# Kernel optimization log

Measured on AMD Instinct MI355X. Metric: run time of the kernel, lower is better.

Reference implementation:

```python
import jax, jax.numpy as jnp
import numpy as np

H, ND, RD, VD = 16, 128, 64, 128  # heads, nope/rope/v head dims
EPS = 1e-6


def rmsnorm(x, g):
    return x * jax.lax.rsqrt(jnp.mean(x * x, axis=-1, keepdims=True) + EPS) * g


def apply_rope(x, cos, sin):
    # x: [B,T,h,D]; cos/sin: [1,T,1,D/2]; interleaved pair rotation
    x1, x2 = x[..., 0::2], x[..., 1::2]
    o1 = x1 * cos - x2 * sin
    o2 = x1 * sin + x2 * cos
    return jnp.stack([o1, o2], axis=-1).reshape(x.shape)


def setup_inputs() -> dict:
    key = jax.random.key(0)
    ks = jax.random.split(key, 10)
    B, T, D = 2, 2048, 2048
    QR, KVR = 1536, 512
    s = 0.02
    return {
        "x": jax.random.normal(ks[0], (B, T, D), jnp.float32),
        "w_cq": jax.random.normal(ks[1], (D, QR), jnp.float32) * s,
        "g_q": jnp.ones((QR,), jnp.float32),
        "w_ckv": jax.random.normal(ks[2], (D, KVR), jnp.float32) * s,
        "g_kv": jnp.ones((KVR,), jnp.float32),
        "w_dq_nope": jax.random.normal(ks[3], (QR, H * ND), jnp.float32) * s,
        "w_dq_rope": jax.random.normal(ks[4], (QR, H * RD), jnp.float32) * s,
        "w_dk_nope": jax.random.normal(ks[5], (KVR, H * ND), jnp.float32) * s,
        "w_dv": jax.random.normal(ks[6], (KVR, H * VD), jnp.float32) * s,
        "w_k_rope": jax.random.normal(ks[7], (D, RD), jnp.float32) * s,
        "w_out": jax.random.normal(ks[8], (H * VD, D), jnp.float32) * s,
    }


def reference(x, w_cq, g_q, w_ckv, g_kv, w_dq_nope, w_dq_rope,
              w_dk_nope, w_dv, w_k_rope, w_out):
    B, T, D = x.shape
    # low-rank latents + RMSNorm
    q_lat = rmsnorm(x @ w_cq, g_q)          # [B,T,QR]
    kv_lat = rmsnorm(x @ w_ckv, g_kv)        # [B,T,KVR]
    q_nope = (q_lat @ w_dq_nope).reshape(B, T, H, ND)
    q_rope = (q_lat @ w_dq_rope).reshape(B, T, H, RD)
    k_nope = (kv_lat @ w_dk_nope).reshape(B, T, H, ND)
    v = (kv_lat @ w_dv).reshape(B, T, H, VD)
    k_rope = (x @ w_k_rope).reshape(B, T, 1, RD)  # shared across heads
    # RoPE (start_pos = 0, no past_kv)
    pos = jnp.arange(T, dtype=jnp.float32)
    inv_freq = 1.0 / (10000.0 ** (jnp.arange(0, RD, 2, dtype=jnp.float32) / RD))
    ang = pos[:, None] * inv_freq[None, :]               # [T, RD/2]
    cos = jnp.cos(ang)[None, :, None, :]
    sin = jnp.sin(ang)[None, :, None, :]
    q_rope = apply_rope(q_rope, cos, sin)
    k_rope = apply_rope(k_rope, cos, sin)
    k_rope = jnp.broadcast_to(k_rope, (B, T, H, RD))
    q = jnp.concatenate([q_nope, q_rope], axis=-1).transpose(0, 2, 1, 3)  # [B,H,T,ND+RD]
    k = jnp.concatenate([k_nope, k_rope], axis=-1).transpose(0, 2, 1, 3)
    v_t = v.transpose(0, 2, 1, 3)                                        # [B,H,T,VD]
    # causal SDPA, scale = 1/sqrt(head_dim)
    scale = 1.0 / jnp.sqrt(jnp.asarray(ND + RD, jnp.float32))
    scores = jnp.einsum('bhqd,bhkd->bhqk', q, k) * scale
    causal = jnp.tril(jnp.ones((T, T), dtype=bool))
    scores = jnp.where(causal[None, None], scores, -jnp.inf)
    attn = jax.nn.softmax(scores, axis=-1)
    out = jnp.einsum('bhqk,bhkd->bhqd', attn, v_t)
    out = out.transpose(0, 2, 1, 3).reshape(B, T, H * VD) @ w_out        # [B,T,D]
    return out, k, v_t
```

## Files before the change

### kernel.cpp

```cpp
#include <hip/hip_runtime.h>
#include <cstdint>
#include <cstddef>

typedef _Float16 HT;
typedef _Float16 h8 __attribute__((ext_vector_type(8)));
typedef _Float16 h4 __attribute__((ext_vector_type(4)));
typedef float f32x4 __attribute__((ext_vector_type(4)));

constexpr int Tn  = 2048;
constexpr int Dm  = 2048;
constexpr int Hh  = 16;
constexpr int RDc = 64;
constexpr int QRc = 1536;
constexpr int KVRc= 512;
constexpr int BT  = 4096;

#define VWAIT(N) asm volatile("s_waitcnt vmcnt(" #N ")" ::: "memory")
#define SBAR()   __builtin_amdgcn_s_barrier()

__device__ __forceinline__ f32x4 mfma16(h8 a, h8 b, f32x4 c) {
    return __builtin_amdgcn_mfma_f32_16x16x32_f16(a, b, c, 0, 0, 0);
}
__device__ __forceinline__ void gload_lds16(const void* g, void* l) {
    __builtin_amdgcn_global_load_lds(
        (const __attribute__((address_space(1))) unsigned int*)g,
        (__attribute__((address_space(3))) unsigned int*)l, 16, 0, 0);
}

__global__ __launch_bounds__(256)
void cstab_kernel(float2* __restrict__ cs)
{
    const int idx = blockIdx.x * 256 + threadIdx.x;
    const int t = idx >> 5, i = idx & 31;
    const float ang = (float)t * exp2f(-(float)i * (13.287712379549449f / 32.f));
    cs[idx] = make_float2(cosf(ang), sinf(ang));
}

struct WT8 {
    const float* s[8];
    HT* d[8];
    int K[8], N[8], start[8];
};

__global__ __launch_bounds__(256)
void wtrans8_kernel(WT8 p)
{
    __shared__ float Ts[64][65];
    int seg = 0;
    #pragma unroll
    for (int i = 1; i < 8; i++) if ((int)blockIdx.x >= p.start[i]) seg = i;
    const float* src = p.s[seg];
    HT* dst = p.d[seg];
    const int K = p.K[seg], N = p.N[seg];
    const int bx = blockIdx.x - p.start[seg];
    const int nx = N >> 6;
    const int n0 = (bx % nx) * 64, k0 = (bx / nx) * 64;
    const int tid = threadIdx.x;
    {
        const int r = tid >> 2, c0 = (tid & 3) * 16;
        const float* s = src + (size_t)(k0 + r) * N + n0 + c0;
        #pragma unroll
        for (int j = 0; j < 4; j++)
            *reinterpret_cast<f32x4*>(&Ts[r][c0 + j * 4]) = *reinterpret_cast<const f32x4*>(s + j * 4);
    }
    __syncthreads();
    {
        const int c = tid >> 2, kq = (tid & 3) * 16;
        h8 o0, o1;
        #pragma unroll
        for (int j = 0; j < 8; j++) { o0[j] = (HT)Ts[kq + j][c]; o1[j] = (HT)Ts[kq + 8 + j][c]; }
        HT* d = dst + (size_t)(n0 + c) * K + k0 + kq;
        *reinterpret_cast<h8*>(d)     = o0;
        *reinterpret_cast<h8*>(d + 8) = o1;
    }
}

__global__ __launch_bounds__(256)
void convx_kernel(const float* __restrict__ x, HT* __restrict__ x16)
{
    const size_t i = ((size_t)blockIdx.x * 256 + threadIdx.x) * 8;
    f32x4 a = *reinterpret_cast<const f32x4*>(x + i);
    f32x4 b = *reinterpret_cast<const f32x4*>(x + i + 4);
    h8 v;
    #pragma unroll
    for (int j = 0; j < 4; j++) { v[j] = (HT)a[j]; v[4 + j] = (HT)b[j]; }
    *reinterpret_cast<h8*>(x16 + i) = v;
}

template<int EPI>
__global__ __launch_bounds__(256)
void gemm16d(const HT* __restrict__ A, const HT* __restrict__ Bt, const int K,
             HT* __restrict__ o1, HT* __restrict__ o2, HT* __restrict__ o3,
             float* __restrict__ f1, float* __restrict__ f2,
             const float2* __restrict__ cstab)
{
    __shared__ HT As[2][4096];
    __shared__ HT Bs[2][4096];

    const int tid  = threadIdx.x;
    const int lane = tid & 63;
    const int l15  = lane & 15, l4 = lane >> 4;
    const int w    = tid >> 6;
    const int wr   = w >> 1, wc = w & 1;
    const int m0   = blockIdx.y * 128;
    const int n0   = blockIdx.x * 128;

    f32x4 acc[4][4] = {};
    const int nk = K >> 5;

    const int schunk = ((lane & 3) ^ ((lane >> 2) & 3) ^ ((lane >> 4) & 3)) * 8;

#define GSTAGE(as_, bs_, kt_) do {                                             \
    _Pragma("unroll")                                                          \
    for (int i_ = 0; i_ < 2; i_++) {                                           \
        const int row_ = (w * 2 + i_) * 16 + (lane >> 2);                      \
        gload_lds16(A  + (size_t)(m0 + row_) * K + (kt_) + schunk,             \
                    (as_) + (w * 2 + i_) * 512);                               \
        gload_lds16(Bt + (size_t)(n0 + row_) * K + (kt_) + schunk,             \
                    (bs_) + (w * 2 + i_) * 512);                               \
    } } while (0)

    GSTAGE(As[0], Bs[0], 0);

    const int sl = (l4 ^ (l15 & 3) ^ ((l15 >> 2) & 3)) * 8;

    for (int kt = 0; kt < nk; kt++) {
        HT* as = As[kt & 1];
        HT* bs = Bs[kt & 1];
        if (kt + 1 < nk) {
            GSTAGE(As[(kt + 1) & 1], Bs[(kt + 1) & 1], (kt + 1) * 32);
            VWAIT(4);
        } else {
            VWAIT(0);
        }
        SBAR();

        h8 af[4], bf[4];
        #pragma unroll
        for (int f = 0; f < 4; f++)
            af[f] = *reinterpret_cast<const h8*>(&as[(wr * 64 + f * 16 + l15) * 32 + sl]);
        #pragma unroll
        for (int g = 0; g < 4; g++)
            bf[g] = *reinterpret_cast<const h8*>(&bs[(wc * 64 + g * 16 + l15) * 32 + sl]);
        #pragma unroll
        for (int f = 0; f < 4; f++)
            #pragma unroll
            for (int g = 0; g < 4; g++)
                acc[f][g] = mfma16(af[f], bf[g], acc[f][g]);
        SBAR();
    }
#undef GSTAGE

    #pragma unroll
    for (int f = 0; f < 4; f++) {
        #pragma unroll
        for (int g = 0; g < 4; g++) {
            const int row = m0 + wr * 64 + f * 16 + l4 * 4;
            const int col = n0 + wc * 64 + g * 16 + l15;
            if constexpr (EPI == 3) {
                #pragma unroll
                for (int r = 0; r < 4; r++)
                    f1[(size_t)(row + r) * 2048 + col] = acc[f][g][r];
            } else if constexpr (EPI == 0) {
                if (col < 1536) {
                    #pragma unroll
                    for (int r = 0; r < 4; r++)
                        o1[(size_t)(row + r) * 1536 + col] = (HT)acc[f][g][r];
                } else if (col < 2048) {
                    #pragma unroll
                    for (int r = 0; r < 4; r++)
                        o2[(size_t)(row + r) * 512 + (col - 1536)] = (HT)acc[f][g][r];
                } else if (col < 2112) {
                    const int cc = col - 2048;
                    const int i = cc >> 1;
                    const bool odd = cc & 1;
                    #pragma unroll
                    for (int r = 0; r < 4; r++) {
                        const int t = (row + r) & (Tn - 1);
                        const float2 cs = cstab[t * 32 + i];
                        const float v = acc[f][g][r];
                        const float p = __shfl_xor(v, 1);
                        const float ov = odd ? p * cs.y + v * cs.x : v * cs.x - p * cs.y;
                        o3[(size_t)(row + r) * 64 + cc] = (HT)ov;
                    }
                }
            } else if constexpr (EPI == 1) {
                if (col < 2048) {
                    #pragma unroll
                    for (int r = 0; r < 4; r++)
                        o1[(size_t)(row + r) * 2048 + col] = (HT)acc[f][g][r];
                } else {
                    const int cc = col - 2048;
                    const int i = (cc & 63) >> 1;
                    const bool odd = cc & 1;
                    #pragma unroll
                    for (int r = 0; r < 4; r++) {
                        const int t = (row + r) & (Tn - 1);
                        const float2 cs = cstab[t * 32 + i];
                        const float v = acc[f][g][r];
                        const float p = __shfl_xor(v, 1);
                        const float ov = odd ? p * cs.y + v * cs.x : v * cs.x - p * cs.y;
                        o2[(size_t)(row + r) * 1024 + cc] = (HT)ov;
                    }
                }
            } else {
                if (col < 2048) {
                    const int h = col >> 7, d = col & 127;
                    #pragma unroll
                    for (int r = 0; r < 4; r++) {
                        const int rw = row + r;
                        const int b = rw >> 11, t = rw & (Tn - 1);
                        o1[(size_t)rw * 2048 + col] = (HT)acc[f][g][r];
                        f1[((size_t)(b * Hh + h) * Tn + t) * 192 + d] = acc[f][g][r];
                    }
                } else {
                    const int c2 = col - 2048;
                    const int h = c2 >> 7, d = c2 & 127;
                    const int b = row >> 11, t0 = row & (Tn - 1);
                    h4 pk;
                    #pragma unroll
                    for (int r = 0; r < 4; r++) {
                        f2[((size_t)(b * Hh + h) * Tn + t0 + r) * 128 + d] = acc[f][g][r];
                        pk[r] = (HT)acc[f][g][r];
                    }
                    *reinterpret_cast<h4*>(&o3[((size_t)(b * Hh + h) * 128 + d) * Tn + t0]) = pk;
                }
            }
        }
    }
}

__global__ __launch_bounds__(256)
void kropebc_kernel(const HT* __restrict__ kr16, float* __restrict__ out_k)
{
    const int idx = blockIdx.x * 256 + threadIdx.x;
    const int j4 = (idx & 15) * 4;
    const int t  = (idx >> 4) & (Tn - 1);
    const int b  = idx >> 15;
    h4 v = *reinterpret_cast<const h4*>(&kr16[((size_t)(b * Tn + t)) * 64 + j4]);
    f32x4 f;
    #pragma unroll
    for (int r = 0; r < 4; r++) f[r] = (float)v[r];
    #pragma unroll
    for (int h = 0; h < Hh; h++)
        *reinterpret_cast<f32x4*>(&out_k[((size_t)(b * Hh + h) * Tn + t) * 192 + 128 + j4]) = f;
}

__global__ __launch_bounds__(256)
void rmsnorm2_kernel(HT* __restrict__ Xa, const float* __restrict__ ga,
                     HT* __restrict__ Xb, const float* __restrict__ gb)
{
    const int which = blockIdx.y;
    HT* X = which ? Xb : Xa;
    const float* g = which ? gb : ga;
    const int N = which ? 512 : 1536;
    const int row = blockIdx.x;
    HT* x = X + (size_t)row * N;
    float ss = 0.f;
    for (int i = threadIdx.x * 8; i < N; i += 2048) {
        h8 v = *reinterpret_cast<const h8*>(&x[i]);
        #pragma unroll
        for (int j = 0; j < 8; j++) { float f = (float)v[j]; ss += f * f; }
    }
    #pragma unroll
    for (int sh = 32; sh >= 1; sh >>= 1) ss += __shfl_xor(ss, sh);
    __shared__ float red[4];
    if ((threadIdx.x & 63) == 0) red[threadIdx.x >> 6] = ss;
    __syncthreads();
    const float tot = red[0] + red[1] + red[2] + red[3];
    const float scale = rsqrtf(tot / (float)N + 1e-6f);
    for (int i = threadIdx.x * 8; i < N; i += 2048) {
        h8 v = *reinterpret_cast<const h8*>(&x[i]);
        f32x4 g0 = *reinterpret_cast<const f32x4*>(&g[i]);
        f32x4 g1 = *reinterpret_cast<const f32x4*>(&g[i + 4]);
        #pragma unroll
        for (int j = 0; j < 4; j++) { v[j]   = (HT)((float)v[j]   * scale * g0[j]);
                                      v[4+j] = (HT)((float)v[4+j] * scale * g1[j]); }
        *reinterpret_cast<h8*>(&x[i]) = v;
    }
}

__global__ __launch_bounds__(256, 2)
void attn10_kernel(const HT* __restrict__ qn, const HT* __restrict__ qr,
                   const HT* __restrict__ kn, const HT* __restrict__ kr16,
                   const HT* __restrict__ vt, HT* __restrict__ ao)
{
    __shared__ HT Ks_n[2][32 * 128];
    __shared__ HT Ks_r[2][32 * 64];
    __shared__ HT Vs[2][128 * 32];
    __shared__ HT Ps[4][32][40];

    const int tid  = threadIdx.x;
    const int lane = tid & 63;
    const int l15  = lane & 15, l4 = lane >> 4;
    const int w    = tid >> 6;

    const int bid = blockIdx.x;
    const int j   = bid >> 5;
    const int h   = bid & 15;
    const int b   = (bid >> 4) & 1;
    const int thi = 31 - j;

    const size_t bT = (size_t)b * Tn;
    const HT* vt_h = vt + ((size_t)(b * Hh + h) * 128) * Tn;

    const int qw0 = j   * 64 + w * 16;
    const int qw1 = thi * 64 + w * 16;

    h8 aq0[6], aq1[6];
    {
        const HT sc = (HT)(0.07216878364870323f * 1.4426950408889634f);
        const size_t rq0 = bT + qw0 + l15;
        const HT* pn = qn + rq0 * 2048 + h * 128 + l4 * 8;
        #pragma unroll
        for (int f = 0; f < 4; f++) aq0[f] = *reinterpret_cast<const h8*>(pn + f * 32) * sc;
        const HT* pr = qr + rq0 * 1024 + h * 64 + l4 * 8;
        aq0[4] = *reinterpret_cast<const h8*>(pr) * sc;
        aq0[5] = *reinterpret_cast<const h8*>(pr + 32) * sc;
        const size_t rq1 = bT + qw1 + l15;
        const HT* pn1 = qn + rq1 * 2048 + h * 128 + l4 * 8;
        #pragma unroll
        for (int f = 0; f < 4; f++) aq1[f] = *reinterpret_cast<const h8*>(pn1 + f * 32) * sc;
        const HT* pr1 = qr + rq1 * 1024 + h * 64 + l4 * 8;
        aq1[4] = *reinterpret_cast<const h8*>(pr1) * sc;
        aq1[5] = *reinterpret_cast<const h8*>(pr1 + 32) * sc;
    }

    f32x4 o0[8] = {}, o1[8] = {};
    float m0v[4] = {-1e30f, -1e30f, -1e30f, -1e30f};
    float m1v[4] = {-1e30f, -1e30f, -1e30f, -1e30f};
    float l0v[4] = {0.f, 0.f, 0.f, 0.f};
    float l1v[4] = {0.f, 0.f, 0.f, 0.f};

#define STAGE(sl_, kb_) do {                                                    \
    _Pragma("unroll")                                                           \
    for (int jj = 0; jj < 2; jj++) {                                            \
        const int cc = w * 2 + jj;                                              \
        const int r_ = cc * 4 + (lane >> 4);                                    \
        const int cl = (l15 & 8) | ((l15 & 7) ^ (r_ & 7));                      \
        gload_lds16(kn + (bT + (kb_) + r_) * 2048 + h * 128 + cl * 8,           \
                    &Ks_n[sl_][cc * 512]);                                      \
    }                                                                           \
    {                                                                           \
        const int r_ = w * 8 + (lane >> 3);                                     \
        const int cl = (lane & 7) ^ (r_ & 7);                                   \
        gload_lds16(kr16 + (bT + (kb_) + r_) * 64 + cl * 8,                     \
                    &Ks_r[sl_][w * 512]);                                       \
    }                                                                           \
    _Pragma("unroll")                                                           \
    for (int jj = 0; jj < 2; jj++) {                                            \
        const int cc = w * 2 + jj;                                              \
        const int d_ = cc * 16 + (lane >> 2);                                   \
        const int cl = (lane & 3) ^ (d_ & 3);                                   \
        gload_lds16(vt_h + (size_t)d_ * Tn + (kb_) + cl * 8,                    \
                    &Vs[sl_][cc * 512]);                                        \
    } } while (0)

#define SMX(sv, mv, lv, ov, qwx, prow)                                          \
{                                                                               \
    float a_[4][2]; float mxr_[4]; bool ok_ = true;                             \
    _Pragma("unroll")                                                           \
    for (int r = 0; r < 4; r++) {                                               \
        const int qrow = (qwx) + l4 * 4 + r;                                    \
        _Pragma("unroll")                                                       \
        for (int c = 0; c < 2; c++)                                             \
            a_[r][c] = (kb + c * 16 + l15 <= qrow) ? sv[c][r] : -1e30f;         \
        mxr_[r] = fmaxf(a_[r][0], a_[r][1]);                                    \
        ok_ = ok_ && (mxr_[r] <= mv[r] + 8.f);                                  \
    }                                                                           \
    if (__builtin_expect((bool)__all(ok_), 1)) {                                \
        _Pragma("unroll")                                                       \
        for (int r = 0; r < 4; r++) {                                           \
            float rs = 0.f;                                                     \
            _Pragma("unroll")                                                   \
            for (int c = 0; c < 2; c++) {                                       \
                const float e = __builtin_exp2f(a_[r][c] - mv[r]);              \
                rs += e;                                                        \
                Ps[w][(prow) + l4 * 4 + r][c * 16 + l15] = (HT)e;               \
            }                                                                   \
            lv[r] += rs;                                                        \
        }                                                                       \
    } else {                                                                    \
        float al_[4];                                                           \
        _Pragma("unroll")                                                       \
        for (int r = 0; r < 4; r++) {                                           \
            float mx = mxr_[r];                                                 \
            _Pragma("unroll")                                                   \
            for (int sh = 1; sh < 16; sh <<= 1) mx = fmaxf(mx, __shfl_xor(mx, sh)); \
            const float mn = fmaxf(mv[r], mx);                                  \
            al_[r] = __builtin_exp2f(mv[r] - mn);                               \
            mv[r] = mn;                                                         \
            float rs = 0.f;                                                     \
            _Pragma("unroll")                                                   \
            for (int c = 0; c < 2; c++) {                                       \
                const float e = __builtin_exp2f(a_[r][c] - mn);                 \
                rs += e;                                                        \
                Ps[w][(prow) + l4 * 4 + r][c * 16 + l15] = (HT)e;               \
            }                                                                   \
            lv[r] = lv[r] * al_[r] + rs;                                        \
        }                                                                       \
        _Pragma("unroll")                                                       \
        for (int g = 0; g < 8; g++)                                             \
            _Pragma("unroll")                                                   \
            for (int r = 0; r < 4; r++) ov[g][r] *= al_[r];                     \
    }                                                                           \
}

#define KBODY(ACT0)                                                             \
{                                                                               \
    f32x4 s0[2] = {}, s1[2] = {};                                               \
    __builtin_amdgcn_s_setprio(1);                                              \
    _Pragma("unroll")                                                           \
    for (int c = 0; c < 2; c++) {                                               \
        const int kr = c * 16 + l15;                                            \
        const int sw = (kr & 7) << 4;                                           \
        const char* kbase = (const char*)&Ks_n[sl][0] + kr * 256;               \
        const char* rbase = (const char*)&Ks_r[sl][0] + kr * 128;               \
        const h8 br0 = *(const h8*)(rbase + ((l4 * 16) ^ sw));                  \
        const h8 br1 = *(const h8*)(rbase + ((64 + l4 * 16) ^ sw));             \
        _Pragma("unroll")                                                       \
        for (int f = 0; f < 4; f++) {                                           \
            const h8 kf = *(const h8*)(kbase + ((f * 64 + l4 * 16) ^ sw));      \
            s1[c] = mfma16(aq1[f], kf, s1[c]);                                  \
            if (ACT0) s0[c] = mfma16(aq0[f], kf, s0[c]);                        \
        }                                                                       \
        s1[c] = mfma16(aq1[4], br0, s1[c]);                                     \
        s1[c] = mfma16(aq1[5], br1, s1[c]);                                     \
        if (ACT0) { s0[c] = mfma16(aq0[4], br0, s0[c]);                         \
                    s0[c] = mfma16(aq0[5], br1, s0[c]); }                       \
    }                                                                           \
    __builtin_amdgcn_s_setprio(0);                                              \
    SMX(s1, m1v, l1v, o1, qw1, 16);                                             \
    if (ACT0) SMX(s0, m0v, l0v, o0, qw0, 0);                                    \
    const h8 ap1 = *reinterpret_cast<const h8*>(&Ps[w][16 + l15][l4 * 8]);      \
    h8 ap0 = ap1;                                                               \
    if (ACT0) ap0 = *reinterpret_cast<const h8*>(&Ps[w][l15][l4 * 8]);          \
    __builtin_amdgcn_s_setprio(1);                                              \
    _Pragma("unroll")                                                           \
    for (int g = 0; g < 8; g++) {                                               \
        const int d = g * 16 + l15;                                             \
        const int swd = (d & 3) << 4;                                           \
        const char* vbase = (const char*)&Vs[sl][0] + d * 64;                   \
        const h8 v0 = *(const h8*)(vbase + ((l4 * 16) ^ swd));                  \
        o1[g] = mfma16(ap1, v0, o1[g]);                                         \
        if (ACT0) o0[g] = mfma16(ap0, v0, o0[g]);                               \
    }                                                                           \
    __builtin_amdgcn_s_setprio(0);                                              \
}

    const int nkb = (thi + 1) * 2;
    STAGE(0, 0);

    for (int t = 0; t < nkb; t++) {
        const int kb = t * 32;
        const int sl = t & 1;
        if (t + 1 < nkb) {
            STAGE(sl ^ 1, kb + 32);
            VWAIT(5);
        } else {
            VWAIT(0);
        }
        SBAR();
        if (kb <= qw0 + 15)      KBODY(1)
        else if (kb <= qw1 + 15) KBODY(0)
        SBAR();
    }
#undef KBODY
#undef SMX
#undef STAGE

    {
        const size_t orow = bT + qw1 + l4 * 4;
        #pragma unroll
        for (int r = 0; r < 4; r++) {
            float rsum = l1v[r];
            #pragma unroll
            for (int sh = 1; sh < 16; sh <<= 1) rsum += __shfl_xor(rsum, sh);
            const float inv = 1.0f / rsum;
            HT* dst = ao + (orow + r) * 2048 + h * 128 + l15;
            #pragma unroll
            for (int g = 0; g < 8; g++) dst[g * 16] = (HT)(o1[g][r] * inv);
        }
    }
    {
        const size_t orow = bT + qw0 + l4 * 4;
        #pragma unroll
        for (int r = 0; r < 4; r++) {
            float rsum = l0v[r];
            #pragma unroll
            for (int sh = 1; sh < 16; sh <<= 1) rsum += __shfl_xor(rsum, sh);
            const float inv = 1.0f / rsum;
            HT* dst = ao + (orow + r) * 2048 + h * 128 + l15;
            #pragma unroll
            for (int g = 0; g < 8; g++) dst[g * 16] = (HT)(o0[g][r] * inv);
        }
    }
}

extern "C" void kernel_launch(void* const* d_in, const int* in_sizes, int n_in,
                              void* d_out, int out_size, void* d_ws, size_t ws_size,
                              hipStream_t stream)
{
    const float* x     = (const float*)d_in[0];
    const float* w_cq  = (const float*)d_in[1];
    const float* g_q   = (const float*)d_in[2];
    const float* w_ckv = (const float*)d_in[3];
    const float* g_kv  = (const float*)d_in[4];
    const float* w_dqn = (const float*)d_in[5];
    const float* w_dqr = (const float*)d_in[6];
    const float* w_dkn = (const float*)d_in[7];
    const float* w_dv  = (const float*)d_in[8];
    const float* w_kr  = (const float*)d_in[9];
    const float* w_out = (const float*)d_in[10];

    char* ws = (char*)d_ws;
    HT* cqT   = (HT*)(ws + 0);
    HT* ckvT  = (HT*)(ws + 6291456);
    HT* krT   = (HT*)(ws + 8388608);
    HT* dqnT  = (HT*)(ws + 8912896);
    HT* dqrT  = (HT*)(ws + 15204352);
    HT* dknT  = (HT*)(ws + 18350080);
    HT* dvT   = (HT*)(ws + 20447232);
    HT* outT  = (HT*)(ws + 22544384);
    HT* cq    = (HT*)(ws + 30932992);
    HT* ckv   = (HT*)(ws + 43515904);
    HT* qn    = (HT*)(ws + 47710208);
    HT* qr    = (HT*)(ws + 64487424);
    HT* kn    = (HT*)(ws + 72876032);
    HT* kr16  = (HT*)(ws + 89653248);
    HT* vt    = (HT*)(ws + 0);
    HT* x16   = qn;
    HT* ao    = qn;

    float* out_o = (float*)d_out;
    float* out_k = out_o + (size_t)BT * Dm;
    float* out_v = out_k + (size_t)2 * Hh * Tn * 192;
    float2* cstab = (float2*)out_v;

    const dim3 blk(256);

    cstab_kernel<<<dim3(256), blk, 0, stream>>>(cstab);

    WT8 wt;
    wt.s[0]=w_cq;  wt.d[0]=cqT;  wt.K[0]=2048; wt.N[0]=1536;
    wt.s[1]=w_ckv; wt.d[1]=ckvT; wt.K[1]=2048; wt.N[1]=512;
    wt.s[2]=w_kr;  wt.d[2]=krT;  wt.K[2]=2048; wt.N[2]=64;
    wt.s[3]=w_dqn; wt.d[3]=dqnT; wt.K[3]=1536; wt.N[3]=2048;
    wt.s[4]=w_dqr; wt.d[4]=dqrT; wt.K[4]=1536; wt.N[4]=1024;
    wt.s[5]=w_dkn; wt.d[5]=dknT; wt.K[5]=512;  wt.N[5]=2048;
    wt.s[6]=w_dv;  wt.d[6]=dvT;  wt.K[6]=512;  wt.N[6]=2048;
    wt.s[7]=w_out; wt.d[7]=outT; wt.K[7]=2048; wt.N[7]=2048;
    {
        int acc = 0;
        for (int i = 0; i < 8; i++) {
            wt.start[i] = acc;
            acc += (wt.N[i] >> 6) * (wt.K[i] >> 6);
        }
        wtrans8_kernel<<<dim3(acc), blk, 0, stream>>>(wt);
    }

    convx_kernel<<<dim3(4096), blk, 0, stream>>>(x, x16);

    gemm16d<0><<<dim3(17, BT/128), blk, 0, stream>>>(x16, cqT, Dm,
        cq, ckv, kr16, nullptr, nullptr, cstab);
    kropebc_kernel<<<dim3(256), blk, 0, stream>>>(kr16, out_k);

    rmsnorm2_kernel<<<dim3(BT, 2), blk, 0, stream>>>(cq, g_q, ckv, g_kv);

    gemm16d<1><<<dim3(24, BT/128), blk, 0, stream>>>(cq, dqnT, QRc,
        qn, qr, nullptr, nullptr, nullptr, cstab);
    gemm16d<2><<<dim3(32, BT/128), blk, 0, stream>>>(ckv, dknT, KVRc,
        kn, nullptr, vt, out_k, out_v, nullptr);

    attn10_kernel<<<dim3(512), blk, 0, stream>>>(qn, qr, kn, kr16, vt, ao);

    gemm16d<3><<<dim3(16, BT/128), blk, 0, stream>>>(ao, outT, Dm,
        nullptr, nullptr, nullptr, out_o, nullptr, nullptr);
}
```

Before: 340.8 us.

## Merge prep kernels into one launch, fuse k_rope broadcast into GEMM, retune V swizzle

Folds the cos/sin table, weight transpose and x-to-fp16 conversion into a single prep kernel dispatched by block-index range, which removes two launches. It also writes the roped k_rope broadcast to all 16 heads of the fp32 output directly from the first GEMM epilogue, so the separate broadcast kernel goes away. The V tile LDS swizzle in attention now uses (d>>1)&3 instead of d&3 to change the bank-conflict pattern. The new epilogue stores are scalar and strided rather than vectorized, and they lengthen the first GEMM.

```diff
diff --git a/kernel.cpp b/kernel.cpp
--- a/kernel.cpp
+++ b/kernel.cpp
@@ -27,35 +27,49 @@
         (__attribute__((address_space(3))) unsigned int*)l, 16, 0, 0);
 }
 
-__global__ __launch_bounds__(256)
-void cstab_kernel(float2* __restrict__ cs)
-{
-    const int idx = blockIdx.x * 256 + threadIdx.x;
-    const int t = idx >> 5, i = idx & 31;
-    const float ang = (float)t * exp2f(-(float)i * (13.287712379549449f / 32.f));
-    cs[idx] = make_float2(cosf(ang), sinf(ang));
-}
-
-struct WT8 {
+struct PrepArgs {
     const float* s[8];
     HT* d[8];
     int K[8], N[8], start[8];
+    float2* cs;
+    const float* x;
+    HT* x16;
 };
 
 __global__ __launch_bounds__(256)
-void wtrans8_kernel(WT8 p)
+void prep_kernel(PrepArgs p)
 {
     __shared__ float Ts[64][65];
+    const int bid = blockIdx.x;
+    const int tid = threadIdx.x;
+
+    if (bid < 256) {
+        const int idx = bid * 256 + tid;
+        const int t = idx >> 5, i = idx & 31;
+        const float ang = (float)t * exp2f(-(float)i * (13.287712379549449f / 32.f));
+        p.cs[idx] = make_float2(cosf(ang), sinf(ang));
+        return;
+    }
+    if (bid >= 4000) {
+        const size_t i = ((size_t)(bid - 4000) * 256 + tid) * 8;
+        f32x4 a = *reinterpret_cast<const f32x4*>(p.x + i);
+        f32x4 b = *reinterpret_cast<const f32x4*>(p.x + i + 4);
+        h8 v;
+        #pragma unroll
+        for (int j = 0; j < 4; j++) { v[j] = (HT)a[j]; v[4 + j] = (HT)b[j]; }
+        *reinterpret_cast<h8*>(p.x16 + i) = v;
+        return;
+    }
+    const int bx0 = bid - 256;
     int seg = 0;
     #pragma unroll
-    for (int i = 1; i < 8; i++) if ((int)blockIdx.x >= p.start[i]) seg = i;
+    for (int i = 1; i < 8; i++) if (bx0 >= p.start[i]) seg = i;
     const float* src = p.s[seg];
     HT* dst = p.d[seg];
     const int K = p.K[seg], N = p.N[seg];
-    const int bx = blockIdx.x - p.start[seg];
+    const int bx = bx0 - p.start[seg];
     const int nx = N >> 6;
     const int n0 = (bx % nx) * 64, k0 = (bx / nx) * 64;
-    const int tid = threadIdx.x;
     {
         const int r = tid >> 2, c0 = (tid & 3) * 16;
         const float* s = src + (size_t)(k0 + r) * N + n0 + c0;
@@ -73,18 +87,6 @@
         *reinterpret_cast<h8*>(d)     = o0;
         *reinterpret_cast<h8*>(d + 8) = o1;
     }
-}
-
-__global__ __launch_bounds__(256)
-void convx_kernel(const float* __restrict__ x, HT* __restrict__ x16)
-{
-    const size_t i = ((size_t)blockIdx.x * 256 + threadIdx.x) * 8;
-    f32x4 a = *reinterpret_cast<const f32x4*>(x + i);
-    f32x4 b = *reinterpret_cast<const f32x4*>(x + i + 4);
-    h8 v;
-    #pragma unroll
-    for (int j = 0; j < 4; j++) { v[j] = (HT)a[j]; v[4 + j] = (HT)b[j]; }
-    *reinterpret_cast<h8*>(x16 + i) = v;
 }
 
 template<int EPI>
@@ -176,12 +178,17 @@
                     const bool odd = cc & 1;
                     #pragma unroll
                     for (int r = 0; r < 4; r++) {
-                        const int t = (row + r) & (Tn - 1);
+                        const int rw = row + r;
+                        const int t = rw & (Tn - 1);
+                        const int b = rw >> 11;
                         const float2 cs = cstab[t * 32 + i];
                         const float v = acc[f][g][r];
                         const float p = __shfl_xor(v, 1);
                         const float ov = odd ? p * cs.y + v * cs.x : v * cs.x - p * cs.y;
-                        o3[(size_t)(row + r) * 64 + cc] = (HT)ov;
+                        o3[(size_t)rw * 64 + cc] = (HT)ov;
+                        #pragma unroll
+                        for (int hh = 0; hh < Hh; hh++)
+                            f1[((size_t)(b * Hh + hh) * Tn + t) * 192 + 128 + cc] = ov;
                     }
                 }
             } else if constexpr (EPI == 1) {
@@ -228,22 +235,6 @@
             }
         }
     }
-}
-
-__global__ __launch_bounds__(256)
-void kropebc_kernel(const HT* __restrict__ kr16, float* __restrict__ out_k)
-{
-    const int idx = blockIdx.x * 256 + threadIdx.x;
-    const int j4 = (idx & 15) * 4;
-    const int t  = (idx >> 4) & (Tn - 1);
-    const int b  = idx >> 15;
-    h4 v = *reinterpret_cast<const h4*>(&kr16[((size_t)(b * Tn + t)) * 64 + j4]);
-    f32x4 f;
-    #pragma unroll
-    for (int r = 0; r < 4; r++) f[r] = (float)v[r];
-    #pragma unroll
-    for (int h = 0; h < Hh; h++)
-        *reinterpret_cast<f32x4*>(&out_k[((size_t)(b * Hh + h) * Tn + t) * 192 + 128 + j4]) = f;
 }
 
 __global__ __launch_bounds__(256)
@@ -351,7 +342,7 @@
     for (int jj = 0; jj < 2; jj++) {                                            \
         const int cc = w * 2 + jj;                                              \
         const int d_ = cc * 16 + (lane >> 2);                                   \
-        const int cl = (lane & 3) ^ (d_ & 3);                                   \
+        const int cl = (lane & 3) ^ ((d_ >> 1) & 3);                            \
         gload_lds16(vt_h + (size_t)d_ * Tn + (kb_) + cl * 8,                    \
                     &Vs[sl_][cc * 512]);                                        \
     } } while (0)
@@ -439,7 +430,7 @@
     _Pragma("unroll")                                                           \
     for (int g = 0; g < 8; g++) {                                               \
         const int d = g * 16 + l15;                                             \
-        const int swd = (d & 3) << 4;                                           \
+        const int swd = ((d >> 1) & 3) << 4;                                    \
         const char* vbase = (const char*)&Vs[sl][0] + d * 64;                   \
         const h8 v0 = *(const h8*)(vbase + ((l4 * 16) ^ swd));                  \
         o1[g] = mfma16(ap1, v0, o1[g]);                                         \
@@ -539,31 +530,27 @@
 
     const dim3 blk(256);
 
-    cstab_kernel<<<dim3(256), blk, 0, stream>>>(cstab);
-
-    WT8 wt;
-    wt.s[0]=w_cq;  wt.d[0]=cqT;  wt.K[0]=2048; wt.N[0]=1536;
-    wt.s[1]=w_ckv; wt.d[1]=ckvT; wt.K[1]=2048; wt.N[1]=512;
-    wt.s[2]=w_kr;  wt.d[2]=krT;  wt.K[2]=2048; wt.N[2]=64;
-    wt.s[3]=w_dqn; wt.d[3]=dqnT; wt.K[3]=1536; wt.N[3]=2048;
-    wt.s[4]=w_dqr; wt.d[4]=dqrT; wt.K[4]=1536; wt.N[4]=1024;
-    wt.s[5]=w_dkn; wt.d[5]=dknT; wt.K[5]=512;  wt.N[5]=2048;
-    wt.s[6]=w_dv;  wt.d[6]=dvT;  wt.K[6]=512;  wt.N[6]=2048;
-    wt.s[7]=w_out; wt.d[7]=outT; wt.K[7]=2048; wt.N[7]=2048;
+    PrepArgs pa;
+    pa.s[0]=w_cq;  pa.d[0]=cqT;  pa.K[0]=2048; pa.N[0]=1536;
+    pa.s[1]=w_ckv; pa.d[1]=ckvT; pa.K[1]=2048; pa.N[1]=512;
+    pa.s[2]=w_kr;  pa.d[2]=krT;  pa.K[2]=2048; pa.N[2]=64;
+    pa.s[3]=w_dqn; pa.d[3]=dqnT; pa.K[3]=1536; pa.N[3]=2048;
+    pa.s[4]=w_dqr; pa.d[4]=dqrT; pa.K[4]=1536; pa.N[4]=1024;
+    pa.s[5]=w_dkn; pa.d[5]=dknT; pa.K[5]=512;  pa.N[5]=2048;
+    pa.s[6]=w_dv;  pa.d[6]=dvT;  pa.K[6]=512;  pa.N[6]=2048;
+    pa.s[7]=w_out; pa.d[7]=outT; pa.K[7]=2048; pa.N[7]=2048;
     {
         int acc = 0;
         for (int i = 0; i < 8; i++) {
-            wt.start[i] = acc;
-            acc += (wt.N[i] >> 6) * (wt.K[i] >> 6);
+            pa.start[i] = acc;
+            acc += (pa.N[i] >> 6) * (pa.K[i] >> 6);
         }
-        wtrans8_kernel<<<dim3(acc), blk, 0, stream>>>(wt);
-    }
-
-    convx_kernel<<<dim3(4096), blk, 0, stream>>>(x, x16);
+    }
+    pa.cs = cstab; pa.x = x; pa.x16 = x16;
+    prep_kernel<<<dim3(8096), blk, 0, stream>>>(pa);
 
     gemm16d<0><<<dim3(17, BT/128), blk, 0, stream>>>(x16, cqT, Dm,
-        cq, ckv, kr16, nullptr, nullptr, cstab);
-    kropebc_kernel<<<dim3(256), blk, 0, stream>>>(kr16, out_k);
+        cq, ckv, kr16, out_k, nullptr, cstab);
 
     rmsnorm2_kernel<<<dim3(BT, 2), blk, 0, stream>>>(cq, g_q, ckv, g_kv);
 
```

Measured after the change: 383.7 us. 1.13x slower.
